# Optimization experiments

Hardware: AMD Instinct MI355X
Metric: run time of the kernel (lower is better)

Reference implementation:

```python
import jax, jax.numpy as jnp
import numpy as np

DIM = 512
NUM_HEADS = 8
HEAD_DIM = DIM // NUM_HEADS          # 64
KEY_DIM = int(HEAD_DIM * 0.5)        # 32
H_QKV = DIM + NUM_HEADS * KEY_DIM * 2  # 1024
SCALE = KEY_DIM ** -0.5
EPS = 1e-5


def bn(x, gamma, beta, mean, var):
    # inference-mode BatchNorm2d over channel axis 1 of NCHW
    inv = gamma / jnp.sqrt(var + EPS)
    return x * inv[None, :, None, None] + (beta - mean * inv)[None, :, None, None]


def conv1x1(x, w):
    # w: [out, in] (1x1 conv collapsed); x: NCHW
    return jnp.einsum('bchw,oc->bohw', x, w)


def dwconv3x3(x, w):
    # depthwise 3x3, 'same' padding; w: [C,1,3,3]
    return jax.lax.conv_general_dilated(
        x, w, window_strides=(1, 1), padding='SAME',
        feature_group_count=x.shape[1],
        dimension_numbers=('NCHW', 'OIHW', 'NCHW'))


def setup_inputs() -> dict:
    key = jax.random.key(0)
    ks = jax.random.split(key, 16)
    B, C, H, W = 8, DIM, 40, 40
    f = jax.random.normal
    inp = {
        'x': f(ks[0], (B, C, H, W), jnp.float32),
        'qkv_w': f(ks[1], (H_QKV, DIM), jnp.float32) * (1.0 / np.sqrt(DIM)),
        'qkv_gamma': 1.0 + 0.1 * f(ks[2], (H_QKV,), jnp.float32),
        'qkv_beta': 0.1 * f(ks[3], (H_QKV,), jnp.float32),
        'qkv_mean': 0.1 * f(ks[4], (H_QKV,), jnp.float32),
        'qkv_var': jax.random.uniform(ks[5], (H_QKV,), jnp.float32) + 0.5,
        'pe_w': f(ks[6], (DIM, 1, 3, 3), jnp.float32) * (1.0 / 3.0),
        'pe_gamma': 1.0 + 0.1 * f(ks[7], (DIM,), jnp.float32),
        'pe_beta': 0.1 * f(ks[8], (DIM,), jnp.float32),
        'pe_mean': 0.1 * f(ks[9], (DIM,), jnp.float32),
        'pe_var': jax.random.uniform(ks[10], (DIM,), jnp.float32) + 0.5,
        'proj_w': f(ks[11], (DIM, DIM), jnp.float32) * (1.0 / np.sqrt(DIM)),
        'proj_gamma': 1.0 + 0.1 * f(ks[12], (DIM,), jnp.float32),
        'proj_beta': 0.1 * f(ks[13], (DIM,), jnp.float32),
        'proj_mean': 0.1 * f(ks[14], (DIM,), jnp.float32),
        'proj_var': jax.random.uniform(ks[15], (DIM,), jnp.float32) + 0.5,
    }
    return inp


def reference(x, qkv_w, qkv_gamma, qkv_beta, qkv_mean, qkv_var,
              pe_w, pe_gamma, pe_beta, pe_mean, pe_var,
              proj_w, proj_gamma, proj_beta, proj_mean, proj_var):
    B, C, H, W = x.shape
    N = H * W
    qkv = bn(conv1x1(x, qkv_w), qkv_gamma, qkv_beta, qkv_mean, qkv_var)
    qkv = qkv.reshape(B, NUM_HEADS, KEY_DIM * 2 + HEAD_DIM, N)
    q = qkv[:, :, :KEY_DIM]                    # [B,h,kd,N]
    k = qkv[:, :, KEY_DIM:2 * KEY_DIM]         # [B,h,kd,N]
    v = qkv[:, :, 2 * KEY_DIM:]                # [B,h,hd,N]
    # attn = q^T @ k * scale -> [B,h,N,N], softmax over last dim
    attn = jnp.einsum('bhkn,bhkm->bhnm', q, k) * SCALE
    attn = jax.nn.softmax(attn, axis=-1)
    # out = v @ attn^T -> [B,h,hd,N]
    out = jnp.einsum('bhdm,bhnm->bhdn', v, attn).reshape(B, C, H, W)
    pe = bn(dwconv3x3(v.reshape(B, C, H, W), pe_w), pe_gamma, pe_beta, pe_mean, pe_var)
    y = out + pe
    y = bn(conv1x1(y, proj_w), proj_gamma, proj_beta, proj_mean, proj_var)
    return y
```

## Files before the change

### kernel.cpp

```cpp
#include <hip/hip_runtime.h>
#include <hip/hip_bf16.h>

#define EPS 1e-5f
#define SCALE 0.17677669529663687f
#define QSCALE 0.25500526817095634f

typedef __attribute__((ext_vector_type(8))) short bf16x8;
typedef __attribute__((ext_vector_type(4))) float f32x4;
typedef __attribute__((ext_vector_type(8))) unsigned short u16x8;

__device__ __forceinline__ unsigned short f2bf(float x) {
  union { float f; unsigned int u; } a; a.f = x;
  unsigned int r = a.u + 0x7FFFu + ((a.u >> 16) & 1u);
  return (unsigned short)(r >> 16);
}
__device__ __forceinline__ float bf2f(unsigned short u) {
  union { unsigned int u; float f; } a; a.u = ((unsigned int)u) << 16;
  return a.f;
}

__device__ __forceinline__ float fexp2(float x) {
#if __has_builtin(__builtin_amdgcn_exp2f)
  return __builtin_amdgcn_exp2f(x);
#else
  float r; asm("v_exp_f32 %0, %1" : "=v"(r) : "v"(x)); return r;
#endif
}

__device__ __forceinline__ void gload_lds16(const void* g, void* l) {
  __builtin_amdgcn_global_load_lds(
      (const __attribute__((address_space(1))) unsigned int*)g,
      (__attribute__((address_space(3))) unsigned int*)l, 16, 0, 0);
}

__device__ __forceinline__ unsigned int pack_bf_trunc(float a, float b) {
  return __builtin_amdgcn_perm(__float_as_uint(b), __float_as_uint(a), 0x07060302u);
}

__global__ __launch_bounds__(256) void cast_w_kernel(
    const float* __restrict__ qw, const float* __restrict__ pw,
    short* __restrict__ wq, short* __restrict__ wp) {
  int idx = blockIdx.x * 256 + threadIdx.x;
  const float4* src;
  ushort4* dst;
  if (idx < 131072) {
    src = (const float4*)qw + idx;
    dst = (ushort4*)wq + idx;
  } else {
    src = (const float4*)pw + (idx - 131072);
    dst = (ushort4*)wp + (idx - 131072);
  }
  float4 v = *src;
  ushort4 u;
  u.x = f2bf(v.x); u.y = f2bf(v.y); u.z = f2bf(v.z); u.w = f2bf(v.w);
  *dst = u;
}

__global__ __launch_bounds__(256) void transpose_cast_kernel(
    const float* __restrict__ X, short* __restrict__ XT) {
  __shared__ unsigned short T[64][72];
  const int b = blockIdx.z, c0 = blockIdx.x * 64, n0 = blockIdx.y * 64;
  const int t = threadIdx.x, nl = t & 63, w = t >> 6;
#pragma unroll
  for (int ci = 0; ci < 16; ++ci) {
    int cl = ci * 4 + w;
    T[nl][cl] = f2bf(X[((size_t)(b * 512 + c0 + cl)) * 1600 + n0 + nl]);
  }
  __syncthreads();
  const int n2 = t >> 2, cg = (t & 3) * 16;
  unsigned short* o = (unsigned short*)XT + ((size_t)(b * 1600 + n0 + n2)) * 512 + c0 + cg;
  *(u16x8*)&o[0] = *(const u16x8*)&T[n2][cg];
  *(u16x8*)&o[8] = *(const u16x8*)&T[n2][cg + 8];
}

__global__ __launch_bounds__(256) void transpose16_kernel(
    const short* __restrict__ S, short* __restrict__ D) {
  __shared__ unsigned short T[64][72];
  const int b = blockIdx.z, c0 = blockIdx.x * 64, n0 = blockIdx.y * 64;
  const int t = threadIdx.x, nl = t & 63, w = t >> 6;
  const unsigned short* Sp = (const unsigned short*)S;
#pragma unroll
  for (int ci = 0; ci < 16; ++ci) {
    int cl = ci * 4 + w;
    T[nl][cl] = Sp[((size_t)(b * 512 + c0 + cl)) * 1600 + n0 + nl];
  }
  __syncthreads();
  const int n2 = t >> 2, cg = (t & 3) * 16;
  unsigned short* o = (unsigned short*)D + ((size_t)(b * 1600 + n0 + n2)) * 512 + c0 + cg;
  *(u16x8*)&o[0] = *(const u16x8*)&T[n2][cg];
  *(u16x8*)&o[8] = *(const u16x8*)&T[n2][cg + 8];
}

__global__ __launch_bounds__(256) void qkv_mfma_kernel(
    const short* __restrict__ XT, const short* __restrict__ WQ,
    const float* __restrict__ gamma, const float* __restrict__ beta,
    const float* __restrict__ mean, const float* __restrict__ var,
    short* __restrict__ qT, short* __restrict__ kT,
    short* __restrict__ vb, short* __restrict__ vp) {
  __shared__ __align__(16) unsigned short As[128 * 32];
  __shared__ __align__(16) unsigned short Bs[128 * 32];

  const int t = threadIdx.x, w = t >> 6, lane = t & 63;
  const int quad = lane >> 4, l16 = lane & 15;
  const int wr = w >> 1, wc = w & 1;
  const int ngt = blockIdx.x, h = blockIdx.y;
  const int o0 = h * 128, ng0 = ngt * 128;

  const int srow = lane >> 2;
  const int sseg = (lane & 3) * 8;

  f32x4 acc[4][4];
#pragma unroll
  for (int mi = 0; mi < 4; ++mi)
#pragma unroll
    for (int nj = 0; nj < 4; ++nj) { acc[mi][nj][0]=0.f; acc[mi][nj][1]=0.f; acc[mi][nj][2]=0.f; acc[mi][nj][3]=0.f; }

  for (int kt = 0; kt < 16; ++kt) {
    const int c0 = kt * 32;
    if (kt) __syncthreads();
#pragma unroll
    for (int r = 0; r < 2; ++r) {
      const int row = (r * 4 + w) * 16 + srow;
      gload_lds16(WQ + (size_t)(o0 + row) * 512 + c0 + sseg, As + (r * 4 + w) * 512);
      gload_lds16(XT + (size_t)(ng0 + row) * 512 + c0 + sseg, Bs + (r * 4 + w) * 512);
    }
    __syncthreads();
    bf16x8 af[4], bfr[4];
#pragma unroll
    for (int i = 0; i < 4; ++i) {
      af[i]  = *(const bf16x8*)&As[(wr * 64 + i * 16 + l16) * 32 + quad * 8];
      bfr[i] = *(const bf16x8*)&Bs[(wc * 64 + i * 16 + l16) * 32 + quad * 8];
    }
#pragma unroll
    for (int mi = 0; mi < 4; ++mi)
#pragma unroll
      for (int nj = 0; nj < 4; ++nj)
        acc[mi][nj] = __builtin_amdgcn_mfma_f32_16x16x32_bf16(af[mi], bfr[nj], acc[mi][nj], 0, 0, 0);
  }

  const int ng_base = ng0 + wc * 64;
#pragma unroll
  for (int mi = 0; mi < 4; ++mi) {
    const int ol = wr * 64 + mi * 16 + quad * 4;
    const int ob = o0 + ol;
    float inv[4], add[4];
#pragma unroll
    for (int r = 0; r < 4; ++r) {
      inv[r] = gamma[ob + r] * rsqrtf(var[ob + r] + EPS);
      add[r] = beta[ob + r] - mean[ob + r] * inv[r];
    }
    const int region = wr * 2 + (mi >> 1);
    if (region == 0) {
      const int kk = mi * 16 + quad * 4;
#pragma unroll
      for (int nj = 0; nj < 4; ++nj) {
        int ng = ng_base + nj * 16 + l16;
        int b = ng / 1600, n = ng - b * 1600;
        ushort4 u;
        u.x = f2bf((acc[mi][nj][0] * inv[0] + add[0]) * QSCALE);
        u.y = f2bf((acc[mi][nj][1] * inv[1] + add[1]) * QSCALE);
        u.z = f2bf((acc[mi][nj][2] * inv[2] + add[2]) * QSCALE);
        u.w = f2bf((acc[mi][nj][3] * inv[3] + add[3]) * QSCALE);
        *(ushort4*)&qT[((size_t)(b * 8 + h) * 1600 + n) * 32 + kk] = u;
      }
    } else if (region == 1) {
      const int kk = (mi - 2) * 16 + quad * 4;
#pragma unroll
      for (int nj = 0; nj < 4; ++nj) {
        int ng = ng_base + nj * 16 + l16;
        int b = ng / 1600, n = ng - b * 1600;
        ushort4 u;
        u.x = f2bf(acc[mi][nj][0] * inv[0] + add[0]);
        u.y = f2bf(acc[mi][nj][1] * inv[1] + add[1]);
        u.z = f2bf(acc[mi][nj][2] * inv[2] + add[2]);
        u.w = f2bf(acc[mi][nj][3] * inv[3] + add[3]);
        *(ushort4*)&kT[((size_t)(b * 8 + h) * 1600 + n) * 32 + kk] = u;
      }
    } else {
      const int ch = h * 64 + (ol - 64);
      const int d0 = ol - 64;
#pragma unroll
      for (int nj = 0; nj < 4; ++nj) {
        int ng = ng_base + nj * 16 + l16;
        int b = ng / 1600, n = ng - b * 1600;
        unsigned short val[4];
#pragma unroll
        for (int r = 0; r < 4; ++r)
          val[r] = f2bf(acc[mi][nj][r] * inv[r] + add[r]);
#pragma unroll
        for (int r = 0; r < 4; ++r)
          ((unsigned short*)vb)[((size_t)(b * 512 + ch + r)) * 1600 + n] = val[r];
        unsigned short* dst = (unsigned short*)vp +
            ((size_t)(b * 8 + h) * 200 + (n >> 3)) * 512 + d0 * 8 + (n & 7);
#pragma unroll
        for (int r = 0; r < 4; ++r)
          dst[r * 8] = val[r];
      }
    }
  }
}

__global__ __launch_bounds__(256) void attn_mfma_kernel(
    const short* __restrict__ qT, const short* __restrict__ kT,
    const short* __restrict__ vp, short* __restrict__ ybf) {
  const int N = 1600;
  const int t = threadIdx.x;
  const int w = t >> 6, lane = t & 63, quad = lane >> 4, l16 = lane & 15;
  const int bh = blockIdx.x, b = bh >> 3, h = bh & 7;
  const int n0w = blockIdx.y * 128 + w * 32;
  if (n0w >= 1600) return;

  const unsigned short* qTb = (const unsigned short*)qT + (size_t)bh * N * 32;
  const unsigned short* kTb = (const unsigned short*)kT + (size_t)bh * N * 32;
  const unsigned short* vpb = (const unsigned short*)vp + (size_t)bh * 102400;

  const bf16x8 qf0 = *(const bf16x8*)(qTb + (size_t)(n0w + l16) * 32 + quad * 8);
  const bf16x8 qf1 = *(const bf16x8*)(qTb + (size_t)(n0w + 16 + l16) * 32 + quad * 8);

  f32x4 acc0[4], acc1[4];
#pragma unroll
  for (int i = 0; i < 4; ++i) {
    acc0[i][0]=0.f; acc0[i][1]=0.f; acc0[i][2]=0.f; acc0[i][3]=0.f;
    acc1[i][0]=0.f; acc1[i][1]=0.f; acc1[i][2]=0.f; acc1[i][3]=0.f;
  }
  float den0 = 0.f, den1 = 0.f;
  const f32x4 zero4 = {0.f, 0.f, 0.f, 0.f};

  const int kperm = ((l16 & 12) << 1) + (l16 & 3);
  const unsigned short* kp = kTb + (size_t)kperm * 32 + quad * 8;
  const unsigned short* vq = vpb + (size_t)quad * 512 + l16 * 8;

  bf16x8 ck0 = *(const bf16x8*)kp;
  bf16x8 ck1 = *(const bf16x8*)(kp + 128);
  bf16x8 cv0 = *(const bf16x8*)(vq);
  bf16x8 cv1 = *(const bf16x8*)(vq + 128);
  bf16x8 cv2 = *(const bf16x8*)(vq + 256);
  bf16x8 cv3 = *(const bf16x8*)(vq + 384);
  bf16x8 nk0, nk1, nv0, nv1, nv2, nv3;

#define ATTN_BODY(NXT, CK0, CK1, CV0, CV1, CV2, CV3, NK0, NK1, NV0, NV1, NV2, NV3) \
  { \
    const int nx_ = (NXT) < 50 ? (NXT) : 0; \
    const unsigned short* kpn_ = kp + (size_t)nx_ * 1024; \
    const unsigned short* vqn_ = vq + (size_t)nx_ * 2048; \
    NK0 = *(const bf16x8*)kpn_; \
    NK1 = *(const bf16x8*)(kpn_ + 128); \
    NV0 = *(const bf16x8*)(vqn_); \
    NV1 = *(const bf16x8*)(vqn_ + 128); \
    NV2 = *(const bf16x8*)(vqn_ + 256); \
    NV3 = *(const bf16x8*)(vqn_ + 384); \
    f32x4 s0_ = __builtin_amdgcn_mfma_f32_16x16x32_bf16(CK0, qf0, zero4, 0, 0, 0); \
    f32x4 s1_ = __builtin_amdgcn_mfma_f32_16x16x32_bf16(CK1, qf0, zero4, 0, 0, 0); \
    f32x4 t0_ = __builtin_amdgcn_mfma_f32_16x16x32_bf16(CK0, qf1, zero4, 0, 0, 0); \
    f32x4 t1_ = __builtin_amdgcn_mfma_f32_16x16x32_bf16(CK1, qf1, zero4, 0, 0, 0); \
    float a0_ = fexp2(s0_[0]), a1_ = fexp2(s0_[1]), a2_ = fexp2(s0_[2]), a3_ = fexp2(s0_[3]); \
    float a4_ = fexp2(s1_[0]), a5_ = fexp2(s1_[1]), a6_ = fexp2(s1_[2]), a7_ = fexp2(s1_[3]); \
    float b0_ = fexp2(t0_[0]), b1_ = fexp2(t0_[1]), b2_ = fexp2(t0_[2]), b3_ = fexp2(t0_[3]); \
    float b4_ = fexp2(t1_[0]), b5_ = fexp2(t1_[1]), b6_ = fexp2(t1_[2]), b7_ = fexp2(t1_[3]); \
    den0 += ((a0_ + a1_) + (a2_ + a3_)) + ((a4_ + a5_) + (a6_ + a7_)); \
    den1 += ((b0_ + b1_) + (b2_ + b3_)) + ((b4_ + b5_) + (b6_ + b7_)); \
    union { bf16x8 v; uint4 u; } pk0_, pk1_; \
    pk0_.u.x = pack_bf_trunc(a0_, a1_); pk0_.u.y = pack_bf_trunc(a2_, a3_); \
    pk0_.u.z = pack_bf_trunc(a4_, a5_); pk0_.u.w = pack_bf_trunc(a6_, a7_); \
    pk1_.u.x = pack_bf_trunc(b0_, b1_); pk1_.u.y = pack_bf_trunc(b2_, b3_); \
    pk1_.u.z = pack_bf_trunc(b4_, b5_); pk1_.u.w = pack_bf_trunc(b6_, b7_); \
    acc0[0] = __builtin_amdgcn_mfma_f32_16x16x32_bf16(pk0_.v, CV0, acc0[0], 0, 0, 0); \
    acc1[0] = __builtin_amdgcn_mfma_f32_16x16x32_bf16(pk1_.v, CV0, acc1[0], 0, 0, 0); \
    acc0[1] = __builtin_amdgcn_mfma_f32_16x16x32_bf16(pk0_.v, CV1, acc0[1], 0, 0, 0); \
    acc1[1] = __builtin_amdgcn_mfma_f32_16x16x32_bf16(pk1_.v, CV1, acc1[1], 0, 0, 0); \
    acc0[2] = __builtin_amdgcn_mfma_f32_16x16x32_bf16(pk0_.v, CV2, acc0[2], 0, 0, 0); \
    acc1[2] = __builtin_amdgcn_mfma_f32_16x16x32_bf16(pk1_.v, CV2, acc1[2], 0, 0, 0); \
    acc0[3] = __builtin_amdgcn_mfma_f32_16x16x32_bf16(pk0_.v, CV3, acc0[3], 0, 0, 0); \
    acc1[3] = __builtin_amdgcn_mfma_f32_16x16x32_bf16(pk1_.v, CV3, acc1[3], 0, 0, 0); \
  }

#pragma unroll 1
  for (int mt2 = 0; mt2 < 25; ++mt2) {
    ATTN_BODY(2 * mt2 + 1, ck0, ck1, cv0, cv1, cv2, cv3, nk0, nk1, nv0, nv1, nv2, nv3);
    ATTN_BODY(2 * mt2 + 2, nk0, nk1, nv0, nv1, nv2, nv3, ck0, ck1, cv0, cv1, cv2, cv3);
  }
#undef ATTN_BODY

  den0 += __shfl_xor(den0, 16, 64);
  den0 += __shfl_xor(den0, 32, 64);
  den1 += __shfl_xor(den1, 16, 64);
  den1 += __shfl_xor(den1, 32, 64);
  const float rden0 = 1.f / den0;
  const float rden1 = 1.f / den1;
  float dv0[4], dv1[4];
#pragma unroll
  for (int r = 0; r < 4; ++r) {
    dv0[r] = __shfl(rden0, quad * 4 + r, 64);
    dv1[r] = __shfl(rden1, quad * 4 + r, 64);
  }

  unsigned short* yb = (unsigned short*)ybf + ((size_t)b * 512 + h * 64) * N;
#pragma unroll
  for (int i = 0; i < 4; ++i) {
    const size_t rowo = (size_t)(i * 16 + l16) * N;
    ushort4 o4;
    o4.x = f2bf(acc0[i][0] * dv0[0]);
    o4.y = f2bf(acc0[i][1] * dv0[1]);
    o4.z = f2bf(acc0[i][2] * dv0[2]);
    o4.w = f2bf(acc0[i][3] * dv0[3]);
    *(ushort4*)&yb[rowo + n0w + quad * 4] = o4;
    o4.x = f2bf(acc1[i][0] * dv1[0]);
    o4.y = f2bf(acc1[i][1] * dv1[1]);
    o4.z = f2bf(acc1[i][2] * dv1[2]);
    o4.w = f2bf(acc1[i][3] * dv1[3]);
    *(ushort4*)&yb[rowo + n0w + 16 + quad * 4] = o4;
  }
}

__global__ __launch_bounds__(256) void pe_kernel(
    const short* __restrict__ Ybf, const short* __restrict__ VB,
    const float* __restrict__ pw,
    const float* __restrict__ gamma, const float* __restrict__ beta,
    const float* __restrict__ mean, const float* __restrict__ var,
    short* __restrict__ YB) {
  __shared__ __align__(16) unsigned short V[4 * 42 * 56];
  __shared__ float wlds[36];
  __shared__ float invs[4], adds[4];

  const int t = threadIdx.x;
  const int b = blockIdx.y, c0 = blockIdx.x * 4;

  const u16x8 z = {0, 0, 0, 0, 0, 0, 0, 0};
  for (int k = t; k < 1176; k += 256)
    *(u16x8*)&V[k * 8] = z;
  if (t < 36) wlds[t] = pw[c0 * 9 + t];
  if (t < 4) {
    int c = c0 + t;
    float inv = gamma[c] * rsqrtf(var[c] + EPS);
    invs[t] = inv;
    adds[t] = beta[c] - mean[c] * inv;
  }
  __syncthreads();

  for (int u = t; u < 800; u += 256) {
    int ch = u / 200, j = u - ch * 200;
    int row = j / 5, col8 = (j - row * 5) * 8;
    u16x8 d = *(const u16x8*)((const unsigned short*)VB +
        ((size_t)(b * 512 + c0 + ch) * 1600 + row * 40 + col8));
    *(u16x8*)&V[ch * 2352 + (row + 1) * 56 + 8 + col8] = d;
  }
  __syncthreads();

#pragma unroll 1
  for (int k = 0; k < 25; ++k) {
    int o = k * 256 + t;
    int ch = o / 1600, n = o - ch * 1600;
    int hh = n / 40, ww = n - hh * 40;
    const unsigned short* Vc = &V[ch * 2352 + (hh + 1) * 56 + 8 + ww];
    const float* wk = &wlds[ch * 9];
    float s = 0.f;
#pragma unroll
    for (int dy = 0; dy < 3; ++dy)
#pragma unroll
      for (int dx = 0; dx < 3; ++dx)
        s += wk[dy * 3 + dx] * bf2f(Vc[(dy - 1) * 56 + (dx - 1)]);
    size_t idx = (size_t)(b * 512 + c0 + ch) * 1600 + n;
    float val = bf2f(((const unsigned short*)Ybf)[idx]) + s * invs[ch] + adds[ch];
    YB[idx] = (short)f2bf(val);
  }
}

__global__ __launch_bounds__(256) void proj_mfma_kernel(
    const short* __restrict__ YT, const short* __restrict__ WP,
    const float* __restrict__ gamma, const float* __restrict__ beta,
    const float* __restrict__ mean, const float* __restrict__ var,
    float* __restrict__ OUT) {
  __shared__ __align__(16) unsigned short As[64 * 32];
  __shared__ __align__(16) unsigned short Bs[128 * 32];

  const int t = threadIdx.x, w = t >> 6, lane = t & 63;
  const int quad = lane >> 4, l16 = lane & 15;
  const int wr = w >> 1, wc = w & 1;
  const int ngt = blockIdx.x;
  const int o0 = blockIdx.y * 64;
  const int ng0 = ngt * 128;

  const int srow = lane >> 2;
  const int sseg = (lane & 3) * 8;

  f32x4 acc[2][4];
#pragma unroll
  for (int mi = 0; mi < 2; ++mi)
#pragma unroll
    for (int nj = 0; nj < 4; ++nj) { acc[mi][nj][0]=0.f; acc[mi][nj][1]=0.f; acc[mi][nj][2]=0.f; acc[mi][nj][3]=0.f; }

  for (int kt = 0; kt < 16; ++kt) {
    const int c0 = kt * 32;
    if (kt) __syncthreads();
    {
      const int row = w * 16 + srow;
      gload_lds16(WP + (size_t)(o0 + row) * 512 + c0 + sseg, As + w * 512);
    }
#pragma unroll
    for (int r = 0; r < 2; ++r) {
      const int row = (r * 4 + w) * 16 + srow;
      gload_lds16(YT + (size_t)(ng0 + row) * 512 + c0 + sseg, Bs + (r * 4 + w) * 512);
    }
    __syncthreads();
    bf16x8 af[2], bfr[4];
#pragma unroll
    for (int i = 0; i < 2; ++i)
      af[i] = *(const bf16x8*)&As[(wr * 32 + i * 16 + l16) * 32 + quad * 8];
#pragma unroll
    for (int i = 0; i < 4; ++i)
      bfr[i] = *(const bf16x8*)&Bs[(wc * 64 + i * 16 + l16) * 32 + quad * 8];
#pragma unroll
    for (int mi = 0; mi < 2; ++mi)
#pragma unroll
      for (int nj = 0; nj < 4; ++nj)
        acc[mi][nj] = __builtin_amdgcn_mfma_f32_16x16x32_bf16(af[mi], bfr[nj], acc[mi][nj], 0, 0, 0);
  }

  const int ng_base = ng0 + wc * 64;
#pragma unroll
  for (int mi = 0; mi < 2; ++mi) {
    const int ob = o0 + wr * 32 + mi * 16 + quad * 4;
    float inv[4], add[4];
#pragma unroll
    for (int r = 0; r < 4; ++r) {
      inv[r] = gamma[ob + r] * rsqrtf(var[ob + r] + EPS);
      add[r] = beta[ob + r] - mean[ob + r] * inv[r];
    }
#pragma unroll
    for (int nj = 0; nj < 4; ++nj) {
      int ng = ng_base + nj * 16 + l16;
      int b = ng / 1600, n = ng - b * 1600;
#pragma unroll
      for (int r = 0; r < 4; ++r)
        OUT[((size_t)(b * 512 + ob + r)) * 1600 + n] = acc[mi][nj][r] * inv[r] + add[r];
    }
  }
}

extern "C" void kernel_launch(void* const* d_in, const int* in_sizes, int n_in,
                              void* d_out, int out_size, void* d_ws, size_t ws_size,
                              hipStream_t stream) {
  const float* x          = (const float*)d_in[0];
  const float* qkv_w      = (const float*)d_in[1];
  const float* qkv_gamma  = (const float*)d_in[2];
  const float* qkv_beta   = (const float*)d_in[3];
  const float* qkv_mean   = (const float*)d_in[4];
  const float* qkv_var    = (const float*)d_in[5];
  const float* pe_w       = (const float*)d_in[6];
  const float* pe_gamma   = (const float*)d_in[7];
  const float* pe_beta    = (const float*)d_in[8];
  const float* pe_mean    = (const float*)d_in[9];
  const float* pe_var     = (const float*)d_in[10];
  const float* proj_w     = (const float*)d_in[11];
  const float* proj_gamma = (const float*)d_in[12];
  const float* proj_beta  = (const float*)d_in[13];
  const float* proj_mean  = (const float*)d_in[14];
  const float* proj_var   = (const float*)d_in[15];
  float* out = (float*)d_out;

  float* ws_a = (float*)d_ws;
  short* ybf_attn = (short*)d_ws;
  short* vp   = ybf_attn + (size_t)6553600;
  short* qT   = (short*)(ws_a + (size_t)6553600);
  short* kT   = qT + (size_t)3276800;
  short* vb   = kT + (size_t)3276800;
  short* xT   = vb + (size_t)6553600;
  short* wq   = xT + (size_t)6553600;
  short* wp   = wq + (size_t)524288;
  short* yT   = xT;
  short* ybf_pe = qT;

  cast_w_kernel<<<768, 256, 0, stream>>>(qkv_w, proj_w, wq, wp);
  {
    dim3 grid(8, 25, 8), block(256);
    transpose_cast_kernel<<<grid, block, 0, stream>>>(x, xT);
  }
  {
    dim3 grid(100, 8), block(256);
    qkv_mfma_kernel<<<grid, block, 0, stream>>>(
        xT, wq, qkv_gamma, qkv_beta, qkv_mean, qkv_var, qT, kT, vb, vp);
  }
  {
    dim3 grid(64, 13), block(256);
    attn_mfma_kernel<<<grid, block, 0, stream>>>(qT, kT, vp, ybf_attn);
  }
  {
    dim3 grid(128, 8), block(256);
    pe_kernel<<<grid, block, 0, stream>>>(
        ybf_attn, vb, pe_w, pe_gamma, pe_beta, pe_mean, pe_var, ybf_pe);
  }
  {
    dim3 grid(8, 25, 8), block(256);
    transpose16_kernel<<<grid, block, 0, stream>>>(ybf_pe, yT);
  }
  {
    dim3 grid(100, 8), block(256);
    proj_mfma_kernel<<<grid, block, 0, stream>>>(
        yT, wp, proj_gamma, proj_beta, proj_mean, proj_var, out);
  }
}
```

Before: 235.7 us.

## Share V tiles across waves via double-buffered LDS staging in attention

The attention kernel now stages V tiles into a double-buffered shared-memory array with direct global-to-LDS loads. All four waves of a block read that one copy, instead of each wave loading V into registers from global memory. K fragments are now loaded directly each iteration without the previous register prefetch. Out-of-range waves in the last block are clamped rather than returning early, so every wave reaches the barriers; those waves redo and rewrite the final rows. The aim is less redundant global/L2 traffic for V, at the cost of a barrier per iteration and K load latency that is no longer hidden by prefetching.

```diff
diff --git a/kernel.cpp b/kernel.cpp
--- a/kernel.cpp
+++ b/kernel.cpp
@@ -204,11 +204,12 @@
     const short* __restrict__ qT, const short* __restrict__ kT,
     const short* __restrict__ vp, short* __restrict__ ybf) {
   const int N = 1600;
+  __shared__ __align__(16) unsigned short Vlds[2][8 * 512];
   const int t = threadIdx.x;
   const int w = t >> 6, lane = t & 63, quad = lane >> 4, l16 = lane & 15;
   const int bh = blockIdx.x, b = bh >> 3, h = bh & 7;
-  const int n0w = blockIdx.y * 128 + w * 32;
-  if (n0w >= 1600) return;
+  int n0w = blockIdx.y * 128 + w * 32;
+  if (n0w > 1568) n0w = 1568;
 
   const unsigned short* qTb = (const unsigned short*)qT + (size_t)bh * N * 32;
   const unsigned short* kTb = (const unsigned short*)kT + (size_t)bh * N * 32;
@@ -228,31 +229,24 @@
 
   const int kperm = ((l16 & 12) << 1) + (l16 & 3);
   const unsigned short* kp = kTb + (size_t)kperm * 32 + quad * 8;
-  const unsigned short* vq = vpb + (size_t)quad * 512 + l16 * 8;
-
-  bf16x8 ck0 = *(const bf16x8*)kp;
-  bf16x8 ck1 = *(const bf16x8*)(kp + 128);
-  bf16x8 cv0 = *(const bf16x8*)(vq);
-  bf16x8 cv1 = *(const bf16x8*)(vq + 128);
-  bf16x8 cv2 = *(const bf16x8*)(vq + 256);
-  bf16x8 cv3 = *(const bf16x8*)(vq + 384);
-  bf16x8 nk0, nk1, nv0, nv1, nv2, nv3;
-
-#define ATTN_BODY(NXT, CK0, CK1, CV0, CV1, CV2, CV3, NK0, NK1, NV0, NV1, NV2, NV3) \
+
+#define STAGE_V(BUF, IT) \
   { \
-    const int nx_ = (NXT) < 50 ? (NXT) : 0; \
-    const unsigned short* kpn_ = kp + (size_t)nx_ * 1024; \
-    const unsigned short* vqn_ = vq + (size_t)nx_ * 2048; \
-    NK0 = *(const bf16x8*)kpn_; \
-    NK1 = *(const bf16x8*)(kpn_ + 128); \
-    NV0 = *(const bf16x8*)(vqn_); \
-    NV1 = *(const bf16x8*)(vqn_ + 128); \
-    NV2 = *(const bf16x8*)(vqn_ + 256); \
-    NV3 = *(const bf16x8*)(vqn_ + 384); \
-    f32x4 s0_ = __builtin_amdgcn_mfma_f32_16x16x32_bf16(CK0, qf0, zero4, 0, 0, 0); \
-    f32x4 s1_ = __builtin_amdgcn_mfma_f32_16x16x32_bf16(CK1, qf0, zero4, 0, 0, 0); \
-    f32x4 t0_ = __builtin_amdgcn_mfma_f32_16x16x32_bf16(CK0, qf1, zero4, 0, 0, 0); \
-    f32x4 t1_ = __builtin_amdgcn_mfma_f32_16x16x32_bf16(CK1, qf1, zero4, 0, 0, 0); \
+    _Pragma("unroll") \
+    for (int j_ = 0; j_ < 2; ++j_) { \
+      const int c_ = w * 2 + j_; \
+      const int s_ = c_ >> 2, i_ = c_ & 3; \
+      gload_lds16(vpb + (size_t)((IT) * 8 + s_ * 4 + quad) * 512 + (i_ * 16 + l16) * 8, \
+                  &Vlds[BUF][c_ * 512]); \
+    } \
+  }
+
+#define SUBTILE(K0, K1, V0, V1, V2, V3) \
+  { \
+    f32x4 s0_ = __builtin_amdgcn_mfma_f32_16x16x32_bf16(K0, qf0, zero4, 0, 0, 0); \
+    f32x4 s1_ = __builtin_amdgcn_mfma_f32_16x16x32_bf16(K1, qf0, zero4, 0, 0, 0); \
+    f32x4 t0_ = __builtin_amdgcn_mfma_f32_16x16x32_bf16(K0, qf1, zero4, 0, 0, 0); \
+    f32x4 t1_ = __builtin_amdgcn_mfma_f32_16x16x32_bf16(K1, qf1, zero4, 0, 0, 0); \
     float a0_ = fexp2(s0_[0]), a1_ = fexp2(s0_[1]), a2_ = fexp2(s0_[2]), a3_ = fexp2(s0_[3]); \
     float a4_ = fexp2(s1_[0]), a5_ = fexp2(s1_[1]), a6_ = fexp2(s1_[2]), a7_ = fexp2(s1_[3]); \
     float b0_ = fexp2(t0_[0]), b1_ = fexp2(t0_[1]), b2_ = fexp2(t0_[2]), b3_ = fexp2(t0_[3]); \
@@ -264,22 +258,44 @@
     pk0_.u.z = pack_bf_trunc(a4_, a5_); pk0_.u.w = pack_bf_trunc(a6_, a7_); \
     pk1_.u.x = pack_bf_trunc(b0_, b1_); pk1_.u.y = pack_bf_trunc(b2_, b3_); \
     pk1_.u.z = pack_bf_trunc(b4_, b5_); pk1_.u.w = pack_bf_trunc(b6_, b7_); \
-    acc0[0] = __builtin_amdgcn_mfma_f32_16x16x32_bf16(pk0_.v, CV0, acc0[0], 0, 0, 0); \
-    acc1[0] = __builtin_amdgcn_mfma_f32_16x16x32_bf16(pk1_.v, CV0, acc1[0], 0, 0, 0); \
-    acc0[1] = __builtin_amdgcn_mfma_f32_16x16x32_bf16(pk0_.v, CV1, acc0[1], 0, 0, 0); \
-    acc1[1] = __builtin_amdgcn_mfma_f32_16x16x32_bf16(pk1_.v, CV1, acc1[1], 0, 0, 0); \
-    acc0[2] = __builtin_amdgcn_mfma_f32_16x16x32_bf16(pk0_.v, CV2, acc0[2], 0, 0, 0); \
-    acc1[2] = __builtin_amdgcn_mfma_f32_16x16x32_bf16(pk1_.v, CV2, acc1[2], 0, 0, 0); \
-    acc0[3] = __builtin_amdgcn_mfma_f32_16x16x32_bf16(pk0_.v, CV3, acc0[3], 0, 0, 0); \
-    acc1[3] = __builtin_amdgcn_mfma_f32_16x16x32_bf16(pk1_.v, CV3, acc1[3], 0, 0, 0); \
-  }
+    acc0[0] = __builtin_amdgcn_mfma_f32_16x16x32_bf16(pk0_.v, V0, acc0[0], 0, 0, 0); \
+    acc1[0] = __builtin_amdgcn_mfma_f32_16x16x32_bf16(pk1_.v, V0, acc1[0], 0, 0, 0); \
+    acc0[1] = __builtin_amdgcn_mfma_f32_16x16x32_bf16(pk0_.v, V1, acc0[1], 0, 0, 0); \
+    acc1[1] = __builtin_amdgcn_mfma_f32_16x16x32_bf16(pk1_.v, V1, acc1[1], 0, 0, 0); \
+    acc0[2] = __builtin_amdgcn_mfma_f32_16x16x32_bf16(pk0_.v, V2, acc0[2], 0, 0, 0); \
+    acc1[2] = __builtin_amdgcn_mfma_f32_16x16x32_bf16(pk1_.v, V2, acc1[2], 0, 0, 0); \
+    acc0[3] = __builtin_amdgcn_mfma_f32_16x16x32_bf16(pk0_.v, V3, acc0[3], 0, 0, 0); \
+    acc1[3] = __builtin_amdgcn_mfma_f32_16x16x32_bf16(pk1_.v, V3, acc1[3], 0, 0, 0); \
+  }
+
+  STAGE_V(0, 0);
 
 #pragma unroll 1
-  for (int mt2 = 0; mt2 < 25; ++mt2) {
-    ATTN_BODY(2 * mt2 + 1, ck0, ck1, cv0, cv1, cv2, cv3, nk0, nk1, nv0, nv1, nv2, nv3);
-    ATTN_BODY(2 * mt2 + 2, nk0, nk1, nv0, nv1, nv2, nv3, ck0, ck1, cv0, cv1, cv2, cv3);
-  }
-#undef ATTN_BODY
+  for (int it = 0; it < 25; ++it) {
+    const int cur = it & 1;
+    __syncthreads();
+    if (it + 1 < 25) STAGE_V(cur ^ 1, it + 1);
+
+    const unsigned short* kpm = kp + (size_t)it * 2048;
+    const bf16x8 ka0 = *(const bf16x8*)(kpm);
+    const bf16x8 ka1 = *(const bf16x8*)(kpm + 128);
+    const bf16x8 kb0 = *(const bf16x8*)(kpm + 1024);
+    const bf16x8 kb1 = *(const bf16x8*)(kpm + 1152);
+    const unsigned short* Lc = &Vlds[cur][lane * 8];
+    const bf16x8 va0 = *(const bf16x8*)(Lc);
+    const bf16x8 va1 = *(const bf16x8*)(Lc + 512);
+    const bf16x8 va2 = *(const bf16x8*)(Lc + 1024);
+    const bf16x8 va3 = *(const bf16x8*)(Lc + 1536);
+    const bf16x8 vb0_ = *(const bf16x8*)(Lc + 2048);
+    const bf16x8 vb1_ = *(const bf16x8*)(Lc + 2560);
+    const bf16x8 vb2_ = *(const bf16x8*)(Lc + 3072);
+    const bf16x8 vb3_ = *(const bf16x8*)(Lc + 3584);
+
+    SUBTILE(ka0, ka1, va0, va1, va2, va3);
+    SUBTILE(kb0, kb1, vb0_, vb1_, vb2_, vb3_);
+  }
+#undef SUBTILE
+#undef STAGE_V
 
   den0 += __shfl_xor(den0, 16, 64);
   den0 += __shfl_xor(den0, 32, 64);
```

Result: no change. 238.4 us (+1.1%).
